# Kernel optimization log

Hardware: AMD Instinct MI355X
Metric: run time of the kernel (lower is better)

The kernel has to match this reference:

```python
import jax, jax.numpy as jnp
from jax import lax
import numpy as np

BS = 256       # batch_size
S = 16         # neighbor_samples
HOPS = 2       # context_hops
NREL = 256     # n_relations
HID = 64       # hidden dim
NENT = 100000  # n_entities
NEDGE = 1000000
PS = 8         # path_samples
PLEN = 4       # max_path_len
NPATH = 100000
RD = NREL      # feature_type='id' -> relation_dim == n_relations


def _glorot(k, shape):
    fan_in, fan_out = shape[0], shape[1]
    lim = (6.0 / (fan_in + fan_out)) ** 0.5
    return jax.random.uniform(k, shape, jnp.float32, -lim, lim)


def setup_inputs():
    key = jax.random.key(0)
    ks = jax.random.split(key, 20)
    # relation features: eye(n_relations) + zero padding row (feature_type='id')
    relation_features = jnp.concatenate(
        [jnp.eye(NREL, dtype=jnp.float32), jnp.zeros((1, NREL), jnp.float32)], axis=0)
    inp = {
        'relation_features': relation_features,
        'agg0_w': _glorot(ks[0], (RD, HID)),
        'agg0_b': jnp.zeros((HID,), jnp.float32),
        'agg1_w': _glorot(ks[1], (HID, NREL)),
        'agg1_b': jnp.zeros((NREL,), jnp.float32),
        'lstm_Wih': _glorot(ks[2], (RD, 4 * HID)),
        'lstm_Whh': _glorot(ks[3], (HID, 4 * HID)),
        'lstm_bih': jnp.zeros((4 * HID,), jnp.float32),
        'lstm_bhh': jnp.zeros((4 * HID,), jnp.float32),
        'path_w': _glorot(ks[4], (HID, NREL)),
        'path_b': jnp.zeros((NREL,), jnp.float32),
        'entity_pairs': jax.random.randint(ks[5], (BS, 2), 0, NENT),
        'train_edges': jax.random.randint(ks[6], (BS,), 0, NEDGE),
        'labels': jax.random.randint(ks[7], (BS,), 0, NREL),
        'path_ids': jax.random.randint(ks[8], (BS, PS), 0, NPATH),
        'entity2edges': jax.random.randint(ks[9], (NENT, S), 0, NEDGE),
        'edge2entities': jax.random.randint(ks[10], (NEDGE, 2), 0, NENT),
        'edge2relation': jax.random.randint(ks[11], (NEDGE,), 0, NREL),
        'id2path': jax.random.randint(ks[12], (NPATH, PLEN), 0, NREL + 1),  # NREL = padding id
        'id2length': jax.random.randint(ks[13], (NPATH,), 0, PLEN + 1),
    }
    return inp


def _lstm(x, Wih, Whh, bih, bhh):
    # x: [N, T, D] -> hs: [N, T, H]; torch gate order i, f, g, o
    N = x.shape[0]
    H = Whh.shape[0]
    b = bih + bhh

    def step(carry, xt):
        h, c = carry
        gates = xt @ Wih + h @ Whh + b
        i, f, g, o = jnp.split(gates, 4, axis=-1)
        c = jax.nn.sigmoid(f) * c + jax.nn.sigmoid(i) * jnp.tanh(g)
        h = jax.nn.sigmoid(o) * jnp.tanh(c)
        return (h, c), h

    h0 = jnp.zeros((N, H), x.dtype)
    (_, _), hs = lax.scan(step, (h0, h0), jnp.swapaxes(x, 0, 1))
    return jnp.swapaxes(hs, 0, 1)


def _forward(relation_features, agg0_w, agg0_b, agg1_w, agg1_b,
             lstm_Wih, lstm_Whh, lstm_bih, lstm_bhh, path_w, path_b,
             entity_pairs, train_edges, labels, path_ids,
             entity2edges, edge2entities, edge2relation, id2path, id2length):
    dt = relation_features.dtype
    # ---- _get_neighbors_and_masks ----
    edges_list = [labels]
    masks = []
    te = train_edges[:, None]
    neighbor_entities = entity_pairs
    for i in range(HOPS):
        if i > 0:
            neighbor_entities = edge2entities[edges_list[-1].reshape(-1)].reshape(BS, -1)
        neighbor_edges = entity2edges[neighbor_entities.reshape(-1)].reshape(BS, -1)
        edges_list.append(neighbor_edges)
        masks.append((neighbor_edges != te).astype(dt))
    # ---- gather relation features per hop ----
    edge_vectors = [relation_features[edges_list[0]]]  # [BS, RD]
    for edges in edges_list[1:]:
        rels = edge2relation[edges.reshape(-1)].reshape(edges.shape)
        edge_vectors.append(relation_features[rels])  # [BS, m, RD]
    # ---- iterative mean aggregation ----
    aggs = [(agg0_w, agg0_b, True, jax.nn.relu),
            (agg1_w, agg1_b, False, lambda x: x)]
    for i in range(HOPS):
        w, b, self_inc, act = aggs[i]
        nxt = []
        for hop in range(HOPS - i):
            d = edge_vectors[hop + 1].shape[-1]
            nv = edge_vectors[hop + 1].reshape(BS, -1, 2, S, d)
            mk = masks[hop].reshape(BS, -1, 2, S, 1)
            ev = jnp.mean(nv * mk, axis=-2)   # [BS, m, 2, d]
            out = jnp.mean(ev, axis=-2)       # [BS, m, d]
            if self_inc:
                out = out + edge_vectors[hop].reshape(BS, -1, d)
            nxt.append(act(out @ w + b))
        edge_vectors = nxt
    context_scores = edge_vectors[0].reshape(BS, NREL)
    # ---- path RNN ----
    pids = path_ids.reshape(-1)              # [BS*PS]
    paths = id2path[pids]                    # [BS*PS, PLEN]
    pf = relation_features[paths]            # [BS*PS, PLEN, RD]
    lengths = id2length[pids]                # [BS*PS]
    hs = _lstm(pf, lstm_Wih, lstm_Whh, lstm_bih, lstm_bhh)   # [BS*PS, PLEN, HID]
    padded = jnp.concatenate([jnp.zeros((hs.shape[0], 1, HID), hs.dtype), hs], axis=1)
    last = padded[jnp.arange(hs.shape[0]), lengths]          # [BS*PS, HID]
    p = (last @ path_w + path_b).reshape(BS, PS, NREL)
    path_scores = jnp.mean(p, axis=1)        # path_agg='mean'
    return jax.nn.sigmoid(context_scores + path_scores)


def reference(relation_features, agg0_w, agg0_b, agg1_w, agg1_b,
              lstm_Wih, lstm_Whh, lstm_bih, lstm_bhh, path_w, path_b,
              entity_pairs, train_edges, labels, path_ids,
              entity2edges, edge2entities, edge2relation, id2path, id2length):
    return _forward(relation_features, agg0_w, agg0_b, agg1_w, agg1_b,
                    lstm_Wih, lstm_Whh, lstm_bih, lstm_bhh, path_w, path_b,
                    entity_pairs, train_edges, labels, path_ids,
                    entity2edges, edge2entities, edge2relation, id2path, id2length)
```

## Files before the change

### kernel.cpp

```cpp
#include <hip/hip_runtime.h>
#include <math.h>

#define BS   256
#define S    16
#define NREL 256
#define HID  64
#define PS   8
#define PLEN 4
#define PPB  2
#define HOPBLKS (BS*8)
#define LSTMBLKS (2048/PPB)

__device__ __forceinline__ float sigm(float x){ return 1.0f/(1.0f+expf(-x)); }
__device__ __forceinline__ float lanebc(float v, int l){
  return __uint_as_float(__builtin_amdgcn_readlane(__float_as_uint(v), l));
}

__global__ void __launch_bounds__(256) k_fused(
    const float* __restrict__ agg0_w,
    const float* __restrict__ agg0_b,
    const float* __restrict__ Wih,
    const float* __restrict__ Whh,
    const float* __restrict__ bih, const float* __restrict__ bhh,
    const int* __restrict__ entity_pairs,
    const int* __restrict__ train_edges,
    const int* __restrict__ entity2edges,
    const int* __restrict__ edge2entities,
    const int* __restrict__ edge2relation,
    const int* __restrict__ path_ids, const int* __restrict__ id2path,
    const int* __restrict__ id2length,
    float* __restrict__ ev1m, float* __restrict__ lastws){
  __shared__ float s_g[4][HID];
  int blk = blockIdx.x;
  int tid = threadIdx.x, w = tid >> 6, lane = tid & 63;

  if (blk < HOPBLKS){
    int b = blk >> 3;
    int j = (blk & 7)*4 + w;
    int te   = train_edges[b];
    int ent0 = entity_pairs[b*2 + (j >> 4)];
    int e1   = entity2edges[ent0*S + (j & 15)];
    int rel1 = edge2relation[e1];
    float m0 = (e1 != te) ? (1.0f/32.0f) : 0.0f;
    int r2 = 0; float sc = 0.f;
    if (lane < 32){
      int ent = edge2entities[e1*2 + (lane >> 4)];
      int e2  = entity2edges[ent*S + (lane & 15)];
      r2 = edge2relation[e2];
      sc = (e2 != te) ? (1.0f/32.0f) : 0.0f;
    }
    float acc = agg0_w[rel1*HID + lane];
    #pragma unroll
    for (int t = 0; t < 32; ++t){
      int   rt = __builtin_amdgcn_readlane(r2, t);
      float st = lanebc(sc, t);
      acc += st * agg0_w[rt*HID + lane];
    }
    acc += agg0_b[lane];
    ev1m[(size_t)(b*32 + j)*HID + lane] = m0 * fmaxf(acc, 0.f);
  } else {
    int lb = blk - HOPBLKS;
    int c = w*HID + lane;
    float wreg[HID];
    #pragma unroll
    for (int k = 0; k < HID; ++k) wreg[k] = Whh[k*256 + c];
    float bg = bih[c] + bhh[c];
    for (int p = 0; p < PPB; ++p){
      int n   = lb*PPB + p;
      int pid = path_ids[n];
      int pt0 = id2path[pid*PLEN+0];
      int pt1 = id2path[pid*PLEN+1];
      int pt2 = id2path[pid*PLEN+2];
      int pt3 = id2path[pid*PLEN+3];
      int len = id2length[pid];
      float h = 0.f, cst = 0.f;
      float h1=0.f, h2=0.f, h3=0.f, h4=0.f;
      #pragma unroll
      for (int t = 0; t < PLEN; ++t){
        int pt = (t==0)?pt0:(t==1)?pt1:(t==2)?pt2:pt3;
        float x = (pt < NREL) ? Wih[pt*256 + c] : 0.f;
        float a0=0.f, a1=0.f, a2=0.f, a3=0.f;
        #pragma unroll
        for (int k = 0; k < HID; k += 4){
          a0 += lanebc(h, k  ) * wreg[k  ];
          a1 += lanebc(h, k+1) * wreg[k+1];
          a2 += lanebc(h, k+2) * wreg[k+2];
          a3 += lanebc(h, k+3) * wreg[k+3];
        }
        s_g[w][lane] = ((a0+a1)+(a2+a3)) + x + bg;
        __syncthreads();
        float gi = s_g[0][lane], gf = s_g[1][lane],
              gg = s_g[2][lane], go = s_g[3][lane];
        __syncthreads();
        cst = sigm(gf)*cst + sigm(gi)*tanhf(gg);
        h   = sigm(go)*tanhf(cst);
        if      (t==0) h1=h;
        else if (t==1) h2=h;
        else if (t==2) h3=h;
        else           h4=h;
      }
      float last = 0.f;
      if (len >= 1) last = h1;
      if (len >= 2) last = h2;
      if (len >= 3) last = h3;
      if (len >= 4) last = h4;
      if (w == 0) lastws[(size_t)n*HID + lane] = last;
    }
  }
}

__global__ void k_final(const float* __restrict__ ev1m,
                        const float* __restrict__ lastws,
                        const float* __restrict__ agg1_w,
                        const float* __restrict__ agg1_b,
                        const float* __restrict__ path_w,
                        const float* __restrict__ path_b,
                        float* __restrict__ out){
  int b = blockIdx.x, tid = threadIdx.x;
  __shared__ float s_c[HID], s_al[HID];
  int w = tid >> 6, l = tid & 63;
  if (w == 0){
    float s = 0.f;
    const float* src = ev1m + (size_t)b*32*HID;
    #pragma unroll 8
    for (int j = 0; j < 32; ++j) s += src[j*HID + l];
    s_c[l] = s;
  } else if (w == 1){
    float s = 0.f;
    const float* src = lastws + (size_t)b*PS*HID;
    #pragma unroll
    for (int ps = 0; ps < PS; ++ps) s += src[ps*HID + l];
    s_al[l] = s * 0.125f;
  }
  __syncthreads();
  float acc = agg1_b[tid] + path_b[tid];
  #pragma unroll 8
  for (int k = 0; k < HID; ++k)
    acc += s_c[k]*agg1_w[k*NREL + tid] + s_al[k]*path_w[k*NREL + tid];
  out[b*NREL + tid] = 1.0f/(1.0f+expf(-acc));
}

extern "C" void kernel_launch(void* const* d_in, const int* in_sizes, int n_in,
                              void* d_out, int out_size, void* d_ws, size_t ws_size,
                              hipStream_t stream){
  const float* agg0_w   = (const float*)d_in[1];
  const float* agg0_b   = (const float*)d_in[2];
  const float* agg1_w   = (const float*)d_in[3];
  const float* agg1_b   = (const float*)d_in[4];
  const float* Wih      = (const float*)d_in[5];
  const float* Whh      = (const float*)d_in[6];
  const float* bih      = (const float*)d_in[7];
  const float* bhh      = (const float*)d_in[8];
  const float* path_w   = (const float*)d_in[9];
  const float* path_b   = (const float*)d_in[10];
  const int* entity_pairs  = (const int*)d_in[11];
  const int* train_edges   = (const int*)d_in[12];
  const int* path_ids      = (const int*)d_in[14];
  const int* entity2edges  = (const int*)d_in[15];
  const int* edge2entities = (const int*)d_in[16];
  const int* edge2relation = (const int*)d_in[17];
  const int* id2path       = (const int*)d_in[18];
  const int* id2length     = (const int*)d_in[19];

  float* ws     = (float*)d_ws;
  float* ev1m   = ws;
  float* lastws = ev1m + 524288;

  k_fused<<<HOPBLKS + LSTMBLKS, 256, 0, stream>>>(
      agg0_w, agg0_b, Wih, Whh, bih, bhh,
      entity_pairs, train_edges, entity2edges, edge2entities, edge2relation,
      path_ids, id2path, id2length, ev1m, lastws);
  k_final<<<BS, 256, 0, stream>>>(ev1m, lastws, agg1_w, agg1_b,
                                  path_w, path_b, (float*)d_out);
}
```

Baseline: 131.8 us.

## Use all lanes for hop-2 gathers and split final projection across 64-thread blocks

```diff
diff --git a/kernel.cpp b/kernel.cpp
--- a/kernel.cpp
+++ b/kernel.cpp
@@ -8,8 +8,8 @@
 #define PS   8
 #define PLEN 4
 #define PPB  2
-#define HOPBLKS (BS*8)
-#define LSTMBLKS (2048/PPB)
+#define HOPB  1024
+#define LSTMB (2048/PPB)
 
 __device__ __forceinline__ float sigm(float x){ return 1.0f/(1.0f+expf(-x)); }
 __device__ __forceinline__ float lanebc(float v, int l){
@@ -30,36 +30,43 @@
     const int* __restrict__ path_ids, const int* __restrict__ id2path,
     const int* __restrict__ id2length,
     float* __restrict__ ev1m, float* __restrict__ lastws){
+  __shared__ float s_sc[8][32];
+  __shared__ int   s_r2[8][32];
+  __shared__ int   s_rel1[8];
+  __shared__ float s_m0[8];
   __shared__ float s_g[4][HID];
   int blk = blockIdx.x;
   int tid = threadIdx.x, w = tid >> 6, lane = tid & 63;
 
-  if (blk < HOPBLKS){
-    int b = blk >> 3;
-    int j = (blk & 7)*4 + w;
+  if (blk < HOPB){
+    int b = blk >> 2, q = blk & 3;
+    int jl = tid >> 5, slot = tid & 31;
+    int j  = q*8 + jl;
     int te   = train_edges[b];
     int ent0 = entity_pairs[b*2 + (j >> 4)];
     int e1   = entity2edges[ent0*S + (j & 15)];
-    int rel1 = edge2relation[e1];
-    float m0 = (e1 != te) ? (1.0f/32.0f) : 0.0f;
-    int r2 = 0; float sc = 0.f;
-    if (lane < 32){
-      int ent = edge2entities[e1*2 + (lane >> 4)];
-      int e2  = entity2edges[ent*S + (lane & 15)];
-      r2 = edge2relation[e2];
-      sc = (e2 != te) ? (1.0f/32.0f) : 0.0f;
+    int ent  = edge2entities[e1*2 + (slot >> 4)];
+    int e2   = entity2edges[ent*S + (slot & 15)];
+    int r2   = edge2relation[e2];
+    s_r2[jl][slot] = r2;
+    s_sc[jl][slot] = (e2 != te) ? (1.0f/32.0f) : 0.0f;
+    if (slot == 0){
+      s_rel1[jl] = edge2relation[e1];
+      s_m0[jl]   = (e1 != te) ? (1.0f/32.0f) : 0.0f;
     }
-    float acc = agg0_w[rel1*HID + lane];
+    __syncthreads();
     #pragma unroll
-    for (int t = 0; t < 32; ++t){
-      int   rt = __builtin_amdgcn_readlane(r2, t);
-      float st = lanebc(sc, t);
-      acc += st * agg0_w[rt*HID + lane];
+    for (int rep = 0; rep < 2; ++rep){
+      int jj = w + rep*4;
+      float acc = agg0_w[s_rel1[jj]*HID + lane];
+      #pragma unroll
+      for (int t = 0; t < 32; ++t)
+        acc += s_sc[jj][t] * agg0_w[s_r2[jj][t]*HID + lane];
+      acc += agg0_b[lane];
+      ev1m[(size_t)(b*32 + q*8 + jj)*HID + lane] = s_m0[jj] * fmaxf(acc, 0.f);
     }
-    acc += agg0_b[lane];
-    ev1m[(size_t)(b*32 + j)*HID + lane] = m0 * fmaxf(acc, 0.f);
   } else {
-    int lb = blk - HOPBLKS;
+    int lb = blk - HOPB;
     int c = w*HID + lane;
     float wreg[HID];
     #pragma unroll
@@ -109,35 +116,32 @@
   }
 }
 
-__global__ void k_final(const float* __restrict__ ev1m,
-                        const float* __restrict__ lastws,
-                        const float* __restrict__ agg1_w,
-                        const float* __restrict__ agg1_b,
-                        const float* __restrict__ path_w,
-                        const float* __restrict__ path_b,
-                        float* __restrict__ out){
-  int b = blockIdx.x, tid = threadIdx.x;
-  __shared__ float s_c[HID], s_al[HID];
-  int w = tid >> 6, l = tid & 63;
-  if (w == 0){
-    float s = 0.f;
-    const float* src = ev1m + (size_t)b*32*HID;
-    #pragma unroll 8
-    for (int j = 0; j < 32; ++j) s += src[j*HID + l];
-    s_c[l] = s;
-  } else if (w == 1){
-    float s = 0.f;
-    const float* src = lastws + (size_t)b*PS*HID;
-    #pragma unroll
-    for (int ps = 0; ps < PS; ++ps) s += src[ps*HID + l];
-    s_al[l] = s * 0.125f;
-  }
-  __syncthreads();
-  float acc = agg1_b[tid] + path_b[tid];
+__global__ void __launch_bounds__(64) k_final(
+    const float* __restrict__ ev1m,
+    const float* __restrict__ lastws,
+    const float* __restrict__ agg1_w,
+    const float* __restrict__ agg1_b,
+    const float* __restrict__ path_w,
+    const float* __restrict__ path_b,
+    float* __restrict__ out){
+  int blk = blockIdx.x, l = threadIdx.x;
+  int b = blk >> 2, q = blk & 3;
+  float cs = 0.f;
+  const float* src = ev1m + (size_t)b*32*HID;
+  #pragma unroll 8
+  for (int j = 0; j < 32; ++j) cs += src[j*HID + l];
+  float als = 0.f;
+  const float* sl = lastws + (size_t)b*PS*HID;
+  #pragma unroll
+  for (int ps = 0; ps < PS; ++ps) als += sl[ps*HID + l];
+  als *= 0.125f;
+  int rel = q*64 + l;
+  float acc = agg1_b[rel] + path_b[rel];
   #pragma unroll 8
   for (int k = 0; k < HID; ++k)
-    acc += s_c[k]*agg1_w[k*NREL + tid] + s_al[k]*path_w[k*NREL + tid];
-  out[b*NREL + tid] = 1.0f/(1.0f+expf(-acc));
+    acc += lanebc(cs, k)*agg1_w[k*NREL + rel]
+         + lanebc(als, k)*path_w[k*NREL + rel];
+  out[b*NREL + rel] = 1.0f/(1.0f+expf(-acc));
 }
 
 extern "C" void kernel_launch(void* const* d_in, const int* in_sizes, int n_in,
@@ -166,10 +170,10 @@
   float* ev1m   = ws;
   float* lastws = ev1m + 524288;
 
-  k_fused<<<HOPBLKS + LSTMBLKS, 256, 0, stream>>>(
+  k_fused<<<HOPB + LSTMB, 256, 0, stream>>>(
       agg0_w, agg0_b, Wih, Whh, bih, bhh,
       entity_pairs, train_edges, entity2edges, edge2entities, edge2relation,
       path_ids, id2path, id2length, ev1m, lastws);
-  k_final<<<BS, 256, 0, stream>>>(ev1m, lastws, agg1_w, agg1_b,
-                                  path_w, path_b, (float*)d_out);
+  k_final<<<BS*4, 64, 0, stream>>>(ev1m, lastws, agg1_w, agg1_b,
+                                   path_w, path_b, (float*)d_out);
 }
```

New measurement: 130.2 us. Within noise of the previous version (-1.3%).
